# Optimization experiments

Hardware: AMD Instinct MI355X
Metric: run time of the kernel (lower is better)

The kernel has to match this reference:

```python
import jax, jax.numpy as jnp
import numpy as np

B, NR, NF, NH, NFH, D, HID = 32, 32, 128, 64, 64, 32, 256


def setup_inputs() -> dict:
    key = jax.random.key(0)
    ks = jax.random.split(key, 16)

    def w(k, o, i):
        return (jax.random.normal(k, (o, i), jnp.float32) / np.sqrt(i)).astype(jnp.float32)

    inp = {
        "robot": jax.random.normal(ks[0], (B, NR, D), jnp.float32),
        "frontier": jax.random.normal(ks[1], (B, NF, D), jnp.float32),
        "robot_history": jax.random.normal(ks[2], (B, NH, D), jnp.float32),
        "frontier_history": jax.random.normal(ks[3], (B, NFH, D), jnp.float32),
        "robot_frontier": jax.random.uniform(ks[4], (B, NR, NF), jnp.float32),
        "robot_past": jax.random.uniform(ks[5], (B, NR, NH), jnp.float32),
        "frontier_past": jax.random.uniform(ks[6], (B, NF, NFH), jnp.float32),
        # parameters (torch Linear convention: weight [out, in])
        "Wq": w(ks[7], D, D), "bq": jnp.zeros(D, jnp.float32),
        "Wk": w(ks[8], D, D), "bk": jnp.zeros(D, jnp.float32),
        "Wv": w(ks[9], D, D), "bv": jnp.zeros(D, jnp.float32),
        "Wn1": w(ks[10], HID, 2 * D), "bn1": jnp.zeros(HID, jnp.float32),
        "Wn2": w(ks[11], D, HID), "bn2": jnp.zeros(D, jnp.float32),
        "We1": w(ks[12], HID, 2 * D + 1), "be1": jnp.zeros(HID, jnp.float32),
        "We2": w(ks[13], 1, HID), "be2": jnp.zeros(1, jnp.float32),
    }
    return inp


def reference(robot, frontier, robot_history, frontier_history, robot_frontier,
              robot_past, frontier_past, Wq, bq, Wk, bk, Wv, bv,
              Wn1, bn1, Wn2, bn2, We1, be1, We2, be2):
    def lin(x, W, b):
        return x @ W.T + b

    def nmlp(h):
        return lin(jax.nn.relu(lin(h, Wn1, bn1)), Wn2, bn2)

    def emlp(h):
        return lin(jax.nn.relu(lin(h, We1, be1)), We2, be2)

    def intra(x):  # x: [b, n, D]
        q, k, v = lin(x, Wq, bq), lin(x, Wk, bk), lin(x, Wv, bv)
        e = jax.nn.softmax(jnp.einsum('bnd,bmd->bnm', q, k), axis=-1)
        agg = jnp.einsum('bnm,bmd->bnd', e, v)
        return x + nmlp(jnp.concatenate([x, agg], axis=-1))

    def inter(x, y, dis):  # x: [b,Nx,D], y: [b,Ny,D], dis: [b,Nx,Ny]
        xq, yk, yv = lin(x, Wq, bq), lin(y, Wk, bk), lin(y, Wv, bv)
        b, Nx, _ = x.shape
        Ny = y.shape[1]
        r_i = jnp.broadcast_to(xq[:, :, None, :], (b, Nx, Ny, D))
        f_j = jnp.broadcast_to(yk[:, None, :, :], (b, Nx, Ny, D))
        edge_input = jnp.concatenate([r_i, f_j, dis[..., None]], axis=-1)  # [b,Nx,Ny,65]
        score = emlp(edge_input)[..., 0]                                   # [b,Nx,Ny]
        e = jax.nn.softmax(score, axis=-1)
        agg = jnp.einsum('bnm,bmd->bnd', e, yv)
        x = x + nmlp(jnp.concatenate([x, agg], axis=-1))
        return e, x

    robot = intra(robot)
    frontier = intra(frontier)           # == per-sample intra on [1,Nf,D]
    robot_history = intra(robot_history)
    frontier_history = intra(frontier_history)
    _, robot = inter(robot, robot_history, robot_past)
    _, new_frontier = inter(frontier, frontier_history, frontier_past)
    edge, robot = inter(robot, new_frontier, robot_frontier)
    # original returns the intra-transformed frontier (split_frontier), not new_frontier
    return (robot, frontier, robot_history, frontier_history, edge)
```

## Files before the change

### kernel.cpp

```cpp
#include <hip/hip_runtime.h>

#define BATCH 32
#define NRr 32
#define NFf 128
#define NHh 64
#define NFHh 64
#define TI 4

__device__ __forceinline__ float dot4(float4 a, float4 b) {
    return fmaf(a.x, b.x, fmaf(a.y, b.y, fmaf(a.z, b.z, a.w * b.w)));
}

__global__ __launch_bounds__(256) void intra_kernel(
    const float* __restrict__ robot, const float* __restrict__ frontier,
    const float* __restrict__ rhist, const float* __restrict__ fhist,
    const float* __restrict__ Wq, const float* __restrict__ bq,
    const float* __restrict__ Wk, const float* __restrict__ bk,
    const float* __restrict__ Wv, const float* __restrict__ bv,
    const float* __restrict__ Wn1, const float* __restrict__ bn1,
    const float* __restrict__ Wn2, const float* __restrict__ bn2,
    float* __restrict__ o_robot, float* __restrict__ o_frontier,
    float* __restrict__ o_rh, float* __restrict__ o_fh)
{
    __shared__ __align__(16) float sXc[1024];
    __shared__ __align__(16) float sQ[1024];
    __shared__ __align__(16) float sAgg[1024];
    __shared__ __align__(16) float sS[4096];
    __shared__ __align__(16) float sKT[4128];
    __shared__ __align__(16) float sVT[8192];

    const int blk = blockIdx.x, tid = threadIdx.x;
    const float* xin; float* xout; int N, lgN, b, chunk;
    if (blk < 32)       { xin=robot;    xout=o_robot;    N=32;  lgN=5; b=blk;          chunk=0; }
    else if (blk < 160) { xin=frontier; xout=o_frontier; N=128; lgN=7; b=(blk-32)>>2;  chunk=(blk-32)&3; }
    else if (blk < 224) { xin=rhist;    xout=o_rh;       N=64;  lgN=6; b=(blk-160)>>1; chunk=(blk-160)&1; }
    else                { xin=fhist;    xout=o_fh;       N=64;  lgN=6; b=(blk-224)>>1; chunk=(blk-224)&1; }

    const float* xb = xin + (size_t)b * N * 32;
    const int r0 = chunk << 5;
    const int d = tid & 31;

    {
        int idx = tid;
        #pragma unroll
        for (int it = 0; it < 4; ++it, idx += 256)
            sXc[idx] = xb[(r0 << 5) + idx];
    }

    {
        const float4* wk4 = (const float4*)(Wk + (d << 5));
        const float4* wv4 = (const float4*)(Wv + (d << 5));
        float4 wk[8], wv[8];
        #pragma unroll
        for (int k = 0; k < 8; ++k) { wk[k] = wk4[k]; wv[k] = wv4[k]; }
        const float bkd = bk[d], bvd = bv[d];
        for (int idx = tid; idx < (N << 5); idx += 256) {
            int j = idx >> 5;
            const float4* xr = (const float4*)(xb + (j << 5));
            float aK = bkd, aV = bvd;
            #pragma unroll
            for (int k = 0; k < 8; ++k) {
                float4 xv = xr[k];
                aK += dot4(wk[k], xv);
                aV += dot4(wv[k], xv);
            }
            sKT[d * 129 + j] = aK;
            sVT[(j << 5) + d] = aV;
        }
    }
    __syncthreads();

    {
        const float4* wq4 = (const float4*)(Wq + (d << 5));
        float4 wq[8];
        #pragma unroll
        for (int k = 0; k < 8; ++k) wq[k] = wq4[k];
        const float bqd = bq[d];
        int idx = tid;
        #pragma unroll
        for (int it = 0; it < 4; ++it, idx += 256) {
            int r = idx >> 5;
            const float4* xr = (const float4*)(sXc + (r << 5));
            float a = bqd;
            #pragma unroll
            for (int k = 0; k < 8; ++k) a += dot4(wq[k], xr[k]);
            sQ[idx] = a;
        }
    }
    __syncthreads();

    for (int idx = tid; idx < (N << 5); idx += 256) {
        int r = idx >> lgN, j = idx & (N - 1);
        const float* qr = sQ + (r << 5);
        float a = 0.f;
        #pragma unroll
        for (int e = 0; e < 32; ++e) a = fmaf(qr[e], sKT[e * 129 + j], a);
        sS[idx] = a;
    }
    __syncthreads();

    {
        int r = tid >> 3, l = tid & 7;
        float* row = sS + (r << lgN);
        float m = -1e30f;
        for (int j = l; j < N; j += 8) m = fmaxf(m, row[j]);
        m = fmaxf(m, __shfl_xor(m, 4));
        m = fmaxf(m, __shfl_xor(m, 2));
        m = fmaxf(m, __shfl_xor(m, 1));
        float s = 0.f;
        for (int j = l; j < N; j += 8) { float ev = __expf(row[j] - m); row[j] = ev; s += ev; }
        s += __shfl_xor(s, 4); s += __shfl_xor(s, 2); s += __shfl_xor(s, 1);
        float inv = 1.0f / s;
        for (int j = l; j < N; j += 8) row[j] *= inv;
    }
    __syncthreads();

    {
        int idx = tid;
        #pragma unroll
        for (int it = 0; it < 4; ++it, idx += 256) {
            int r = idx >> 5;
            const float* er = sS + (r << lgN);
            float a = 0.f;
            for (int j = 0; j < N; ++j) a = fmaf(er[j], sVT[(j << 5) + d], a);
            sAgg[idx] = a;
        }
    }
    __syncthreads();

    float* sT = sVT;
    {
        const float4* w14 = (const float4*)(Wn1 + (tid << 6));
        float4 w1r[16];
        #pragma unroll
        for (int k = 0; k < 16; ++k) w1r[k] = w14[k];
        const float b1 = bn1[tid];
        for (int r = 0; r < 32; ++r) {
            const float4* xr = (const float4*)(sXc + (r << 5));
            const float4* ar = (const float4*)(sAgg + (r << 5));
            float a = b1;
            #pragma unroll
            for (int k = 0; k < 8; ++k) a += dot4(w1r[k], xr[k]);
            #pragma unroll
            for (int k = 0; k < 8; ++k) a += dot4(w1r[8 + k], ar[k]);
            sT[(r << 8) + tid] = fmaxf(a, 0.f);
        }
    }
    __syncthreads();

    {
        const int rg = tid >> 5;
        float acc[4] = {0.f, 0.f, 0.f, 0.f};
        #pragma unroll
        for (int hc = 0; hc < 4; ++hc) {
            const float4* w24 = (const float4*)(Wn2 + (d << 8) + (hc << 6));
            float4 w2r[16];
            #pragma unroll
            for (int k = 0; k < 16; ++k) w2r[k] = w24[k];
            #pragma unroll
            for (int p = 0; p < 4; ++p) {
                int r = rg + (p << 3);
                const float4* tr = (const float4*)(sT + (r << 8) + (hc << 6));
                float a = 0.f;
                #pragma unroll
                for (int k = 0; k < 16; ++k) a += dot4(w2r[k], tr[k]);
                acc[p] += a;
            }
        }
        const float b2 = bn2[d];
        #pragma unroll
        for (int p = 0; p < 4; ++p) {
            int r = rg + (p << 3);
            xout[((size_t)b * N << 5) + ((r0 + r) << 5) + d] = sXc[(r << 5) + d] + b2 + acc[p];
        }
    }
}

__global__ __launch_bounds__(256) void pre_y_kernel(
    const float* __restrict__ yA, int NyA, float* __restrict__ wOutA, float* __restrict__ yvOutA, int nBlkA,
    const float* __restrict__ yB, int NyB, float* __restrict__ wOutB, float* __restrict__ yvOutB,
    const float* __restrict__ Wk, const float* __restrict__ bk,
    const float* __restrict__ Wv, const float* __restrict__ bv,
    const float* __restrict__ We1)
{
    __shared__ __align__(16) float sY[256], sK[256];
    const int blk = blockIdx.x, tid = threadIdx.x;
    const float* y; int Ny; float* wOut; float* yvOut; int idx;
    if (blk < nBlkA) { y=yA; Ny=NyA; wOut=wOutA; yvOut=yvOutA; idx=blk; }
    else             { y=yB; Ny=NyB; wOut=wOutB; yvOut=yvOutB; idx=blk-nBlkA; }
    const int chunks = Ny >> 3;
    const int b = idx / chunks, j0 = (idx - b * chunks) << 3;

    sY[tid] = y[((size_t)(b * Ny + j0)) * 32 + tid];
    __syncthreads();

    {
        int jl = tid >> 5, dd = tid & 31;
        const float4* wk4 = (const float4*)(Wk + (dd << 5));
        const float4* wv4 = (const float4*)(Wv + (dd << 5));
        const float4* yr = (const float4*)(sY + (jl << 5));
        float aK = bk[dd], aV = bv[dd];
        #pragma unroll
        for (int k = 0; k < 8; ++k) {
            float4 yv4 = yr[k];
            aK += dot4(wk4[k], yv4);
            aV += dot4(wv4[k], yv4);
        }
        sK[(jl << 5) + dd] = aK;
        yvOut[((size_t)(b * Ny + j0 + jl)) * 32 + dd] = aV;
    }
    __syncthreads();

    {
        const float* w1 = We1 + tid * 65 + 32;
        float acc[8] = {0,0,0,0,0,0,0,0};
        #pragma unroll
        for (int e = 0; e < 32; ++e) {
            float we = w1[e];
            #pragma unroll
            for (int jl = 0; jl < 8; ++jl)
                acc[jl] = fmaf(we, sK[(jl << 5) + e], acc[jl]);
        }
        #pragma unroll
        for (int jl = 0; jl < 8; ++jl)
            wOut[((size_t)(b * Ny + j0 + jl)) * 256 + tid] = acc[jl];
    }
}

__global__ __launch_bounds__(256) void inter_main_kernel(
    const float* __restrict__ xA, int NxA, const float* __restrict__ wA, const float* __restrict__ yvA,
    int NyA, const float* __restrict__ disA, float* __restrict__ outA, float* __restrict__ eA, int nBlkA,
    const float* __restrict__ xB, int NxB, const float* __restrict__ wB, const float* __restrict__ yvB,
    int NyB, const float* __restrict__ disB, float* __restrict__ outB, float* __restrict__ eB,
    const float* __restrict__ Wq, const float* __restrict__ bq,
    const float* __restrict__ We1, const float* __restrict__ be1,
    const float* __restrict__ We2,
    const float* __restrict__ Wn1, const float* __restrict__ bn1,
    const float* __restrict__ Wn2, const float* __restrict__ bn2)
{
    __shared__ __align__(16) float sX[128], sQ[128], sAgg[128];
    __shared__ __align__(16) float sDis[512];
    __shared__ __align__(16) float sU[1024];
    __shared__ __align__(16) float sC[256], sW2[256];
    __shared__ __align__(16) float sS[512];
    __shared__ __align__(16) float sRed[1024];
    __shared__ __align__(16) float sT[1024];

    const int blk = blockIdx.x, tid = threadIdx.x;
    const float* x; int Nx; const float* w; const float* yv; int Ny;
    const float* dis; float* outp; float* ep; int idx;
    if (blk < nBlkA) { x=xA; Nx=NxA; w=wA; yv=yvA; Ny=NyA; dis=disA; outp=outA; ep=eA; idx=blk; }
    else             { x=xB; Nx=NxB; w=wB; yv=yvB; Ny=NyB; dis=disB; outp=outB; ep=eB; idx=blk-nBlkA; }
    const int lgNy = (Ny == 128) ? 7 : 6;
    const int tiles = Nx >> 2;
    const int b = idx / tiles, i0 = (idx - b * tiles) << 2;
    const float* xrow = x + ((size_t)(b * Nx + i0)) * 32;

    if (tid < 128) sX[tid] = xrow[tid];
    for (int k = tid; k < (TI << lgNy); k += 256) {
        int il = k >> lgNy, j = k & (Ny - 1);
        sDis[(il << 7) + j] = dis[((size_t)(b * Nx + i0 + il)) * Ny + j];
    }
    __syncthreads();

    if (tid < 128) {
        int il = tid >> 5, dd = tid & 31;
        const float4* wq4 = (const float4*)(Wq + (dd << 5));
        const float4* xr = (const float4*)(sX + (il << 5));
        float a = bq[dd];
        #pragma unroll
        for (int k = 0; k < 8; ++k) a += dot4(wq4[k], xr[k]);
        sQ[tid] = a;
    }
    __syncthreads();

    {
        const float* w1 = We1 + tid * 65;
        float acc[TI];
        const float b1 = be1[tid];
        #pragma unroll
        for (int il = 0; il < TI; ++il) acc[il] = b1;
        #pragma unroll
        for (int e = 0; e < 32; ++e) {
            float we = w1[e];
            #pragma unroll
            for (int il = 0; il < TI; ++il)
                acc[il] = fmaf(we, sQ[(il << 5) + e], acc[il]);
        }
        #pragma unroll
        for (int il = 0; il < TI; ++il) sU[(il << 8) + tid] = acc[il];
        sC[tid] = w1[64];
        sW2[tid] = We2[tid];
    }
    __syncthreads();

    {
        const int jg = tid >> 5, hh = tid & 31;
        for (int j = jg; j < Ny; j += 8) {
            const float* wr = w + ((size_t)(b * Ny + j)) * 256;
            float dv[TI];
            #pragma unroll
            for (int il = 0; il < TI; ++il) dv[il] = sDis[(il << 7) + j];
            float acc[TI] = {0.f, 0.f, 0.f, 0.f};
            #pragma unroll
            for (int h8 = 0; h8 < 8; ++h8) {
                int h = hh + (h8 << 5);
                float wv_ = wr[h];
                float c = sC[h], w2v = sW2[h];
                #pragma unroll
                for (int il = 0; il < TI; ++il) {
                    float hid = fmaf(c, dv[il], sU[(il << 8) + h] + wv_);
                    acc[il] = fmaf(w2v, fmaxf(hid, 0.f), acc[il]);
                }
            }
            #pragma unroll
            for (int m = 16; m; m >>= 1) {
                #pragma unroll
                for (int il = 0; il < TI; ++il) acc[il] += __shfl_xor(acc[il], m);
            }
            if (hh == 0) {
                #pragma unroll
                for (int il = 0; il < TI; ++il) sS[(il << 7) + j] = acc[il];
            }
        }
    }
    __syncthreads();

    {
        const int il = tid >> 6, lane = tid & 63;
        float m = -1e30f;
        for (int j = lane; j < Ny; j += 64) m = fmaxf(m, sS[(il << 7) + j]);
        #pragma unroll
        for (int msk = 32; msk; msk >>= 1) m = fmaxf(m, __shfl_xor(m, msk));
        float s = 0.f;
        for (int j = lane; j < Ny; j += 64) {
            float ev = __expf(sS[(il << 7) + j] - m);
            sS[(il << 7) + j] = ev; s += ev;
        }
        #pragma unroll
        for (int msk = 32; msk; msk >>= 1) s += __shfl_xor(s, msk);
        float inv = 1.0f / s;
        for (int j = lane; j < Ny; j += 64) sS[(il << 7) + j] *= inv;
    }
    __syncthreads();

    if (ep) {
        for (int k = tid; k < (TI << lgNy); k += 256) {
            int il = k >> lgNy, j = k & (Ny - 1);
            ep[((size_t)(b * Nx + i0 + il)) * Ny + j] = sS[(il << 7) + j];
        }
    }

    {
        const int jg = tid >> 5, dd = tid & 31;
        float p[TI] = {0.f, 0.f, 0.f, 0.f};
        for (int j = jg; j < Ny; j += 8) {
            float v = yv[((size_t)(b * Ny + j)) * 32 + dd];
            #pragma unroll
            for (int il = 0; il < TI; ++il)
                p[il] = fmaf(sS[(il << 7) + j], v, p[il]);
        }
        #pragma unroll
        for (int il = 0; il < TI; ++il) sRed[(jg << 7) + (il << 5) + dd] = p[il];
    }
    __syncthreads();
    if (tid < 128) {
        float a = 0.f;
        #pragma unroll
        for (int jg = 0; jg < 8; ++jg) a += sRed[(jg << 7) + tid];
        sAgg[tid] = a;
    }
    __syncthreads();

    {
        const float4* w14 = (const float4*)(Wn1 + (tid << 6));
        float acc[TI];
        const float b1 = bn1[tid];
        #pragma unroll
        for (int il = 0; il < TI; ++il) acc[il] = b1;
        #pragma unroll
        for (int k = 0; k < 8; ++k) {
            float4 wa = w14[k];
            #pragma unroll
            for (int il = 0; il < TI; ++il)
                acc[il] += dot4(wa, ((const float4*)(sX + (il << 5)))[k]);
        }
        #pragma unroll
        for (int k = 0; k < 8; ++k) {
            float4 wb = w14[8 + k];
            #pragma unroll
            for (int il = 0; il < TI; ++il)
                acc[il] += dot4(wb, ((const float4*)(sAgg + (il << 5)))[k]);
        }
        #pragma unroll
        for (int il = 0; il < TI; ++il) sT[(il << 8) + tid] = fmaxf(acc[il], 0.f);
    }
    __syncthreads();

    {
        const int hg = tid >> 5, dd = tid & 31;
        const float4* w24 = (const float4*)(Wn2 + (dd << 8) + (hg << 5));
        float p[TI] = {0.f, 0.f, 0.f, 0.f};
        #pragma unroll
        for (int k = 0; k < 8; ++k) {
            float4 wv_ = w24[k];
            #pragma unroll
            for (int il = 0; il < TI; ++il)
                p[il] += dot4(wv_, ((const float4*)(sT + (il << 8) + (hg << 5)))[k]);
        }
        #pragma unroll
        for (int il = 0; il < TI; ++il) sRed[(hg << 7) + (il << 5) + dd] = p[il];
    }
    __syncthreads();
    if (tid < 128) {
        int il = tid >> 5, dd = tid & 31;
        float a = bn2[dd] + sX[tid];
        #pragma unroll
        for (int hg = 0; hg < 8; ++hg) a += sRed[(hg << 7) + tid];
        outp[((size_t)(b * Nx + i0 + il)) * 32 + dd] = a;
    }
}

extern "C" void kernel_launch(void* const* d_in, const int* in_sizes, int n_in,
                              void* d_out, int out_size, void* d_ws, size_t ws_size,
                              hipStream_t stream) {
    const float* robot          = (const float*)d_in[0];
    const float* frontier       = (const float*)d_in[1];
    const float* rh             = (const float*)d_in[2];
    const float* fh             = (const float*)d_in[3];
    const float* robot_frontier = (const float*)d_in[4];
    const float* robot_past     = (const float*)d_in[5];
    const float* frontier_past  = (const float*)d_in[6];
    const float* Wq  = (const float*)d_in[7];  const float* bq  = (const float*)d_in[8];
    const float* Wk  = (const float*)d_in[9];  const float* bk  = (const float*)d_in[10];
    const float* Wv  = (const float*)d_in[11]; const float* bv  = (const float*)d_in[12];
    const float* Wn1 = (const float*)d_in[13]; const float* bn1 = (const float*)d_in[14];
    const float* Wn2 = (const float*)d_in[15]; const float* bn2 = (const float*)d_in[16];
    const float* We1 = (const float*)d_in[17]; const float* be1 = (const float*)d_in[18];
    const float* We2 = (const float*)d_in[19];

    float* out = (float*)d_out;
    float* out_robot    = out;
    float* out_frontier = out + 32768;
    float* out_rh       = out + 163840;
    float* out_fh       = out + 229376;
    float* out_edge     = out + 294912;

    float* W = (float*)d_ws;
    float* robot1 = W;
    float* robot2 = W + 32768;
    float* nf     = W + 65536;
    float* w5     = W + 196608;
    float* yv5    = W + 720896;
    float* w6     = W + 786432;
    float* yv6    = W + 1310720;
    float* w7     = W + 1376256;
    float* yv7    = W + 2424832;

    intra_kernel<<<288, 256, 0, stream>>>(robot, frontier, rh, fh,
        Wq, bq, Wk, bk, Wv, bv, Wn1, bn1, Wn2, bn2,
        robot1, out_frontier, out_rh, out_fh);

    pre_y_kernel<<<512, 256, 0, stream>>>(
        out_rh, NHh, w5, yv5, BATCH * NHh / 8,
        out_fh, NFHh, w6, yv6,
        Wk, bk, Wv, bv, We1);

    inter_main_kernel<<<1280, 256, 0, stream>>>(
        robot1, NRr, w5, yv5, NHh, robot_past, robot2, (float*)nullptr, BATCH * (NRr / TI),
        out_frontier, NFf, w6, yv6, NFHh, frontier_past, nf, (float*)nullptr,
        Wq, bq, We1, be1, We2, Wn1, bn1, Wn2, bn2);

    pre_y_kernel<<<512, 256, 0, stream>>>(
        nf, NFf, w7, yv7, BATCH * NFf / 8,
        nf, NFf, w7, yv7,
        Wk, bk, Wv, bv, We1);

    inter_main_kernel<<<256, 256, 0, stream>>>(
        robot2, NRr, w7, yv7, NFf, robot_frontier, out_robot, out_edge, BATCH * (NRr / TI),
        robot2, NRr, w7, yv7, NFf, robot_frontier, out_robot, out_edge,
        Wq, bq, We1, be1, We2, Wn1, bn1, Wn2, bn2);
}
```

Baseline: 223.7 us.

## Fuse key/value precompute into producer kernels and halve inter tile size

Removes both pre_y_kernel launches. The K/V projection and the We1 key contribution are now computed in the epilogue of the kernel that produces each tensor: intra_kernel for the history tensors, inter_main_kernel for new_frontier. The row tile TI drops from 4 to 2, doubling the inter grid and shrinking shared memory per block. The inner score loop now reads weight rows as float4 and keeps per-thread u/c/w2 values in registers. This saves two launches and a re-read of intermediates, at the cost of redundant weight loads per smaller tile and extra tail work in the producer blocks.

New measurement: 381.6 us. 1.71x slower.

```diff
diff --git a/kernel.cpp b/kernel.cpp
--- a/kernel.cpp
+++ b/kernel.cpp
@@ -5,7 +5,7 @@
 #define NFf 128
 #define NHh 64
 #define NFHh 64
-#define TI 4
+#define TI 2
 
 __device__ __forceinline__ float dot4(float4 a, float4 b) {
     return fmaf(a.x, b.x, fmaf(a.y, b.y, fmaf(a.z, b.z, a.w * b.w)));
@@ -19,8 +19,11 @@
     const float* __restrict__ Wv, const float* __restrict__ bv,
     const float* __restrict__ Wn1, const float* __restrict__ bn1,
     const float* __restrict__ Wn2, const float* __restrict__ bn2,
+    const float* __restrict__ We1,
     float* __restrict__ o_robot, float* __restrict__ o_frontier,
-    float* __restrict__ o_rh, float* __restrict__ o_fh)
+    float* __restrict__ o_rh, float* __restrict__ o_fh,
+    float* __restrict__ w5, float* __restrict__ yv5,
+    float* __restrict__ w6, float* __restrict__ yv6)
 {
     __shared__ __align__(16) float sXc[1024];
     __shared__ __align__(16) float sQ[1024];
@@ -31,10 +34,12 @@
 
     const int blk = blockIdx.x, tid = threadIdx.x;
     const float* xin; float* xout; int N, lgN, b, chunk;
+    float* wOut = nullptr; float* yvOut = nullptr;
     if (blk < 32)       { xin=robot;    xout=o_robot;    N=32;  lgN=5; b=blk;          chunk=0; }
     else if (blk < 160) { xin=frontier; xout=o_frontier; N=128; lgN=7; b=(blk-32)>>2;  chunk=(blk-32)&3; }
-    else if (blk < 224) { xin=rhist;    xout=o_rh;       N=64;  lgN=6; b=(blk-160)>>1; chunk=(blk-160)&1; }
-    else                { xin=fhist;    xout=o_fh;       N=64;  lgN=6; b=(blk-224)>>1; chunk=(blk-224)&1; }
+    else if (blk < 224) { xin=rhist;    xout=o_rh;       N=64;  lgN=6; b=(blk-160)>>1; chunk=(blk-160)&1; wOut=w5; yvOut=yv5; }
+    else                { xin=fhist;    xout=o_fh;       N=64;  lgN=6; b=(blk-224)>>1; chunk=(blk-224)&1; wOut=w6; yvOut=yv6; }
+    const bool isPre = (wOut != nullptr);
 
     const float* xb = xin + (size_t)b * N * 32;
     const int r0 = chunk << 5;
@@ -148,6 +153,7 @@
     }
     __syncthreads();
 
+    float* sOut = sQ;
     {
         const int rg = tid >> 5;
         float acc[4] = {0.f, 0.f, 0.f, 0.f};
@@ -171,99 +177,102 @@
         #pragma unroll
         for (int p = 0; p < 4; ++p) {
             int r = rg + (p << 3);
-            xout[((size_t)b * N << 5) + ((r0 + r) << 5) + d] = sXc[(r << 5) + d] + b2 + acc[p];
+            float v = sXc[(r << 5) + d] + b2 + acc[p];
+            xout[((size_t)b * N << 5) + ((r0 + r) << 5) + d] = v;
+            if (isPre) sOut[(r << 5) + d] = v;
+        }
+    }
+
+    if (isPre) {
+        __syncthreads();
+        float* sYK = sKT;
+        {
+            const float4* wk4 = (const float4*)(Wk + (d << 5));
+            const float4* wv4 = (const float4*)(Wv + (d << 5));
+            float4 wk[8], wv[8];
+            #pragma unroll
+            for (int k = 0; k < 8; ++k) { wk[k] = wk4[k]; wv[k] = wv4[k]; }
+            const float bkd = bk[d], bvd = bv[d];
+            const int rg = tid >> 5;
+            #pragma unroll
+            for (int p = 0; p < 4; ++p) {
+                int r = rg + (p << 3);
+                const float4* orow = (const float4*)(sOut + (r << 5));
+                float aK = bkd, aV = bvd;
+                #pragma unroll
+                for (int k = 0; k < 8; ++k) { aK += dot4(wk[k], orow[k]); aV += dot4(wv[k], orow[k]); }
+                sYK[r * 33 + d] = aK;
+                yvOut[(((size_t)(b * N + r0 + r)) << 5) + d] = aV;
+            }
+        }
+        __syncthreads();
+        {
+            const float* w1 = We1 + tid * 65 + 32;
+            #pragma unroll
+            for (int rc = 0; rc < 2; ++rc) {
+                float acc[16];
+                #pragma unroll
+                for (int r2 = 0; r2 < 16; ++r2) acc[r2] = 0.f;
+                #pragma unroll
+                for (int e = 0; e < 32; ++e) {
+                    float we = w1[e];
+                    #pragma unroll
+                    for (int r2 = 0; r2 < 16; ++r2)
+                        acc[r2] = fmaf(we, sYK[(rc * 16 + r2) * 33 + e], acc[r2]);
+                }
+                #pragma unroll
+                for (int r2 = 0; r2 < 16; ++r2)
+                    wOut[(((size_t)(b * N + r0 + rc * 16 + r2)) << 8) + tid] = acc[r2];
+            }
         }
     }
 }
 
-__global__ __launch_bounds__(256) void pre_y_kernel(
-    const float* __restrict__ yA, int NyA, float* __restrict__ wOutA, float* __restrict__ yvOutA, int nBlkA,
-    const float* __restrict__ yB, int NyB, float* __restrict__ wOutB, float* __restrict__ yvOutB,
+__global__ __launch_bounds__(256) void inter_main_kernel(
+    const float* __restrict__ xA, int NxA, const float* __restrict__ wA, const float* __restrict__ yvA,
+    int NyA, const float* __restrict__ disA, float* __restrict__ outA, float* __restrict__ eA,
+    float* __restrict__ wPreA, float* __restrict__ yvPreA, int nBlkA,
+    const float* __restrict__ xB, int NxB, const float* __restrict__ wB, const float* __restrict__ yvB,
+    int NyB, const float* __restrict__ disB, float* __restrict__ outB, float* __restrict__ eB,
+    float* __restrict__ wPreB, float* __restrict__ yvPreB,
+    const float* __restrict__ Wq, const float* __restrict__ bq,
     const float* __restrict__ Wk, const float* __restrict__ bk,
     const float* __restrict__ Wv, const float* __restrict__ bv,
-    const float* __restrict__ We1)
-{
-    __shared__ __align__(16) float sY[256], sK[256];
-    const int blk = blockIdx.x, tid = threadIdx.x;
-    const float* y; int Ny; float* wOut; float* yvOut; int idx;
-    if (blk < nBlkA) { y=yA; Ny=NyA; wOut=wOutA; yvOut=yvOutA; idx=blk; }
-    else             { y=yB; Ny=NyB; wOut=wOutB; yvOut=yvOutB; idx=blk-nBlkA; }
-    const int chunks = Ny >> 3;
-    const int b = idx / chunks, j0 = (idx - b * chunks) << 3;
-
-    sY[tid] = y[((size_t)(b * Ny + j0)) * 32 + tid];
-    __syncthreads();
-
-    {
-        int jl = tid >> 5, dd = tid & 31;
-        const float4* wk4 = (const float4*)(Wk + (dd << 5));
-        const float4* wv4 = (const float4*)(Wv + (dd << 5));
-        const float4* yr = (const float4*)(sY + (jl << 5));
-        float aK = bk[dd], aV = bv[dd];
-        #pragma unroll
-        for (int k = 0; k < 8; ++k) {
-            float4 yv4 = yr[k];
-            aK += dot4(wk4[k], yv4);
-            aV += dot4(wv4[k], yv4);
-        }
-        sK[(jl << 5) + dd] = aK;
-        yvOut[((size_t)(b * Ny + j0 + jl)) * 32 + dd] = aV;
-    }
-    __syncthreads();
-
-    {
-        const float* w1 = We1 + tid * 65 + 32;
-        float acc[8] = {0,0,0,0,0,0,0,0};
-        #pragma unroll
-        for (int e = 0; e < 32; ++e) {
-            float we = w1[e];
-            #pragma unroll
-            for (int jl = 0; jl < 8; ++jl)
-                acc[jl] = fmaf(we, sK[(jl << 5) + e], acc[jl]);
-        }
-        #pragma unroll
-        for (int jl = 0; jl < 8; ++jl)
-            wOut[((size_t)(b * Ny + j0 + jl)) * 256 + tid] = acc[jl];
-    }
-}
-
-__global__ __launch_bounds__(256) void inter_main_kernel(
-    const float* __restrict__ xA, int NxA, const float* __restrict__ wA, const float* __restrict__ yvA,
-    int NyA, const float* __restrict__ disA, float* __restrict__ outA, float* __restrict__ eA, int nBlkA,
-    const float* __restrict__ xB, int NxB, const float* __restrict__ wB, const float* __restrict__ yvB,
-    int NyB, const float* __restrict__ disB, float* __restrict__ outB, float* __restrict__ eB,
-    const float* __restrict__ Wq, const float* __restrict__ bq,
     const float* __restrict__ We1, const float* __restrict__ be1,
     const float* __restrict__ We2,
     const float* __restrict__ Wn1, const float* __restrict__ bn1,
     const float* __restrict__ Wn2, const float* __restrict__ bn2)
 {
-    __shared__ __align__(16) float sX[128], sQ[128], sAgg[128];
-    __shared__ __align__(16) float sDis[512];
-    __shared__ __align__(16) float sU[1024];
+    __shared__ __align__(16) float sX[64], sQ[64], sAgg[64], sOut[64];
+    __shared__ __align__(16) float sYK[66];
+    __shared__ __align__(16) float sDis[256];
+    __shared__ __align__(16) float sU[512];
     __shared__ __align__(16) float sC[256], sW2[256];
-    __shared__ __align__(16) float sS[512];
-    __shared__ __align__(16) float sRed[1024];
-    __shared__ __align__(16) float sT[1024];
+    __shared__ __align__(16) float sS[256];
+    __shared__ __align__(16) float sRed[512];
+    __shared__ __align__(16) float sT[512];
 
     const int blk = blockIdx.x, tid = threadIdx.x;
     const float* x; int Nx; const float* w; const float* yv; int Ny;
-    const float* dis; float* outp; float* ep; int idx;
-    if (blk < nBlkA) { x=xA; Nx=NxA; w=wA; yv=yvA; Ny=NyA; dis=disA; outp=outA; ep=eA; idx=blk; }
-    else             { x=xB; Nx=NxB; w=wB; yv=yvB; Ny=NyB; dis=disB; outp=outB; ep=eB; idx=blk-nBlkA; }
-    const int lgNy = (Ny == 128) ? 7 : 6;
-    const int tiles = Nx >> 2;
-    const int b = idx / tiles, i0 = (idx - b * tiles) << 2;
+    const float* dis; float* outp; float* ep; float* wPre; float* yvPre; int idx;
+    if (blk < nBlkA) { x=xA; Nx=NxA; w=wA; yv=yvA; Ny=NyA; dis=disA; outp=outA; ep=eA; wPre=wPreA; yvPre=yvPreA; idx=blk; }
+    else             { x=xB; Nx=NxB; w=wB; yv=yvB; Ny=NyB; dis=disB; outp=outB; ep=eB; wPre=wPreB; yvPre=yvPreB; idx=blk-nBlkA; }
+    const int tiles = Nx >> 1;
+    const int b = idx / tiles, i0 = (idx - b * tiles) << 1;
     const float* xrow = x + ((size_t)(b * Nx + i0)) * 32;
 
-    if (tid < 128) sX[tid] = xrow[tid];
-    for (int k = tid; k < (TI << lgNy); k += 256) {
-        int il = k >> lgNy, j = k & (Ny - 1);
-        sDis[(il << 7) + j] = dis[((size_t)(b * Nx + i0 + il)) * Ny + j];
-    }
-    __syncthreads();
-
-    if (tid < 128) {
+    if (tid < 64) sX[tid] = xrow[tid];
+    {
+        int per = Ny >> 2;
+        if (tid < (per << 1)) {
+            int il = (tid >= per) ? 1 : 0, jq = tid - il * per;
+            ((float4*)sDis)[(il << 5) + jq] =
+                ((const float4*)(dis + ((size_t)(b * Nx + i0 + il)) * Ny))[jq];
+        }
+    }
+    __syncthreads();
+
+    if (tid < 64) {
         int il = tid >> 5, dd = tid & 31;
         const float4* wq4 = (const float4*)(Wq + (dd << 5));
         const float4* xr = (const float4*)(sX + (il << 5));
@@ -276,19 +285,14 @@
 
     {
         const float* w1 = We1 + tid * 65;
-        float acc[TI];
-        const float b1 = be1[tid];
-        #pragma unroll
-        for (int il = 0; il < TI; ++il) acc[il] = b1;
+        float a0 = be1[tid], a1 = a0;
         #pragma unroll
         for (int e = 0; e < 32; ++e) {
             float we = w1[e];
-            #pragma unroll
-            for (int il = 0; il < TI; ++il)
-                acc[il] = fmaf(we, sQ[(il << 5) + e], acc[il]);
-        }
-        #pragma unroll
-        for (int il = 0; il < TI; ++il) sU[(il << 8) + tid] = acc[il];
+            a0 = fmaf(we, sQ[e], a0);
+            a1 = fmaf(we, sQ[32 + e], a1);
+        }
+        sU[tid] = a0; sU[256 + tid] = a1;
         sC[tid] = w1[64];
         sW2[tid] = We2[tid];
     }
@@ -296,128 +300,148 @@
 
     {
         const int jg = tid >> 5, hh = tid & 31;
+        float ur0[8], ur1[8], cr[8], w2r[8];
+        #pragma unroll
+        for (int k = 0; k < 8; ++k) {
+            int h = (hh << 3) + k;
+            cr[k] = sC[h]; w2r[k] = sW2[h];
+            ur0[k] = sU[h]; ur1[k] = sU[256 + h];
+        }
         for (int j = jg; j < Ny; j += 8) {
-            const float* wr = w + ((size_t)(b * Ny + j)) * 256;
-            float dv[TI];
-            #pragma unroll
-            for (int il = 0; il < TI; ++il) dv[il] = sDis[(il << 7) + j];
-            float acc[TI] = {0.f, 0.f, 0.f, 0.f};
-            #pragma unroll
-            for (int h8 = 0; h8 < 8; ++h8) {
-                int h = hh + (h8 << 5);
-                float wv_ = wr[h];
-                float c = sC[h], w2v = sW2[h];
-                #pragma unroll
-                for (int il = 0; il < TI; ++il) {
-                    float hid = fmaf(c, dv[il], sU[(il << 8) + h] + wv_);
-                    acc[il] = fmaf(w2v, fmaxf(hid, 0.f), acc[il]);
-                }
+            const float4* wr4 = (const float4*)(w + (((size_t)(b * Ny + j)) << 8) + (hh << 3));
+            float4 wa = wr4[0], wb = wr4[1];
+            float dv0 = sDis[j], dv1 = sDis[128 + j];
+            float wv8[8] = {wa.x, wa.y, wa.z, wa.w, wb.x, wb.y, wb.z, wb.w};
+            float a0 = 0.f, a1 = 0.f;
+            #pragma unroll
+            for (int k = 0; k < 8; ++k) {
+                float h0 = fmaf(cr[k], dv0, ur0[k] + wv8[k]);
+                float h1 = fmaf(cr[k], dv1, ur1[k] + wv8[k]);
+                a0 = fmaf(w2r[k], fmaxf(h0, 0.f), a0);
+                a1 = fmaf(w2r[k], fmaxf(h1, 0.f), a1);
             }
             #pragma unroll
             for (int m = 16; m; m >>= 1) {
-                #pragma unroll
-                for (int il = 0; il < TI; ++il) acc[il] += __shfl_xor(acc[il], m);
-            }
-            if (hh == 0) {
-                #pragma unroll
-                for (int il = 0; il < TI; ++il) sS[(il << 7) + j] = acc[il];
-            }
-        }
-    }
-    __syncthreads();
-
-    {
+                a0 += __shfl_xor(a0, m);
+                a1 += __shfl_xor(a1, m);
+            }
+            if (hh == 0) { sS[j] = a0; sS[128 + j] = a1; }
+        }
+    }
+    __syncthreads();
+
+    if (tid < 128) {
         const int il = tid >> 6, lane = tid & 63;
+        float* row = sS + (il << 7);
         float m = -1e30f;
-        for (int j = lane; j < Ny; j += 64) m = fmaxf(m, sS[(il << 7) + j]);
+        for (int j = lane; j < Ny; j += 64) m = fmaxf(m, row[j]);
         #pragma unroll
         for (int msk = 32; msk; msk >>= 1) m = fmaxf(m, __shfl_xor(m, msk));
         float s = 0.f;
-        for (int j = lane; j < Ny; j += 64) {
-            float ev = __expf(sS[(il << 7) + j] - m);
-            sS[(il << 7) + j] = ev; s += ev;
-        }
+        for (int j = lane; j < Ny; j += 64) { float ev = __expf(row[j] - m); row[j] = ev; s += ev; }
         #pragma unroll
         for (int msk = 32; msk; msk >>= 1) s += __shfl_xor(s, msk);
         float inv = 1.0f / s;
-        for (int j = lane; j < Ny; j += 64) sS[(il << 7) + j] *= inv;
+        for (int j = lane; j < Ny; j += 64) row[j] *= inv;
     }
     __syncthreads();
 
     if (ep) {
-        for (int k = tid; k < (TI << lgNy); k += 256) {
-            int il = k >> lgNy, j = k & (Ny - 1);
-            ep[((size_t)(b * Nx + i0 + il)) * Ny + j] = sS[(il << 7) + j];
+        for (int k = tid; k < (TI * 128) && (k >> 7) < TI; k += 256) {
+            int il = k >> 7, j = k & 127;
+            if (j < Ny) ep[((size_t)(b * Nx + i0 + il)) * Ny + j] = sS[(il << 7) + j];
         }
     }
 
     {
         const int jg = tid >> 5, dd = tid & 31;
-        float p[TI] = {0.f, 0.f, 0.f, 0.f};
+        float p0 = 0.f, p1 = 0.f;
         for (int j = jg; j < Ny; j += 8) {
-            float v = yv[((size_t)(b * Ny + j)) * 32 + dd];
-            #pragma unroll
-            for (int il = 0; il < TI; ++il)
-                p[il] = fmaf(sS[(il << 7) + j], v, p[il]);
-        }
-        #pragma unroll
-        for (int il = 0; il < TI; ++il) sRed[(jg << 7) + (il << 5) + dd] = p[il];
-    }
-    __syncthreads();
-    if (tid < 128) {
+            float v = yv[(((size_t)(b * Ny + j)) << 5) + dd];
+            p0 = fmaf(sS[j], v, p0);
+            p1 = fmaf(sS[128 + j], v, p1);
+        }
+        sRed[(jg << 6) + dd] = p0;
+        sRed[(jg << 6) + 32 + dd] = p1;
+    }
+    __syncthreads();
+    if (tid < 64) {
         float a = 0.f;
         #pragma unroll
-        for (int jg = 0; jg < 8; ++jg) a += sRed[(jg << 7) + tid];
+        for (int jg = 0; jg < 8; ++jg) a += sRed[(jg << 6) + tid];
         sAgg[tid] = a;
     }
     __syncthreads();
 
     {
         const float4* w14 = (const float4*)(Wn1 + (tid << 6));
-        float acc[TI];
-        const float b1 = bn1[tid];
-        #pragma unroll
-        for (int il = 0; il < TI; ++il) acc[il] = b1;
+        float a0 = bn1[tid], a1 = a0;
         #pragma unroll
         for (int k = 0; k < 8; ++k) {
             float4 wa = w14[k];
-            #pragma unroll
-            for (int il = 0; il < TI; ++il)
-                acc[il] += dot4(wa, ((const float4*)(sX + (il << 5)))[k]);
+            a0 += dot4(wa, ((const float4*)sX)[k]);
+            a1 += dot4(wa, ((const float4*)(sX + 32))[k]);
         }
         #pragma unroll
         for (int k = 0; k < 8; ++k) {
             float4 wb = w14[8 + k];
-            #pragma unroll
-            for (int il = 0; il < TI; ++il)
-                acc[il] += dot4(wb, ((const float4*)(sAgg + (il << 5)))[k]);
-        }
-        #pragma unroll
-        for (int il = 0; il < TI; ++il) sT[(il << 8) + tid] = fmaxf(acc[il], 0.f);
+            a0 += dot4(wb, ((const float4*)sAgg)[k]);
+            a1 += dot4(wb, ((const float4*)(sAgg + 32))[k]);
+        }
+        sT[tid] = fmaxf(a0, 0.f);
+        sT[256 + tid] = fmaxf(a1, 0.f);
     }
     __syncthreads();
 
     {
         const int hg = tid >> 5, dd = tid & 31;
         const float4* w24 = (const float4*)(Wn2 + (dd << 8) + (hg << 5));
-        float p[TI] = {0.f, 0.f, 0.f, 0.f};
+        float p0 = 0.f, p1 = 0.f;
         #pragma unroll
         for (int k = 0; k < 8; ++k) {
-            float4 wv_ = w24[k];
-            #pragma unroll
-            for (int il = 0; il < TI; ++il)
-                p[il] += dot4(wv_, ((const float4*)(sT + (il << 8) + (hg << 5)))[k]);
-        }
-        #pragma unroll
-        for (int il = 0; il < TI; ++il) sRed[(hg << 7) + (il << 5) + dd] = p[il];
-    }
-    __syncthreads();
-    if (tid < 128) {
+            float4 wv4 = w24[k];
+            p0 += dot4(wv4, ((const float4*)(sT + (hg << 5)))[k]);
+            p1 += dot4(wv4, ((const float4*)(sT + 256 + (hg << 5)))[k]);
+        }
+        sRed[(hg << 6) + dd] = p0;
+        sRed[(hg << 6) + 32 + dd] = p1;
+    }
+    __syncthreads();
+    if (tid < 64) {
         int il = tid >> 5, dd = tid & 31;
         float a = bn2[dd] + sX[tid];
         #pragma unroll
-        for (int hg = 0; hg < 8; ++hg) a += sRed[(hg << 7) + tid];
+        for (int hg = 0; hg < 8; ++hg) a += sRed[(hg << 6) + tid];
         outp[((size_t)(b * Nx + i0 + il)) * 32 + dd] = a;
+        sOut[tid] = a;
+    }
+
+    if (wPre) {
+        __syncthreads();
+        if (tid < 128) {
+            int half = tid >> 6, t = tid & 63;
+            int il = t >> 5, dd = t & 31;
+            const float4* wm4 = (const float4*)((half ? Wv : Wk) + (dd << 5));
+            const float4* orow = (const float4*)(sOut + (il << 5));
+            float a = half ? bv[dd] : bk[dd];
+            #pragma unroll
+            for (int k = 0; k < 8; ++k) a += dot4(wm4[k], orow[k]);
+            if (half) yvPre[(((size_t)(b * Nx + i0 + il)) << 5) + dd] = a;
+            else sYK[il * 33 + dd] = a;
+        }
+        __syncthreads();
+        {
+            const float* w1 = We1 + tid * 65 + 32;
+            float a0 = 0.f, a1 = 0.f;
+            #pragma unroll
+            for (int e = 0; e < 32; ++e) {
+                float we = w1[e];
+                a0 = fmaf(we, sYK[e], a0);
+                a1 = fmaf(we, sYK[33 + e], a1);
+            }
+            wPre[(((size_t)(b * Nx + i0)) << 8) + tid] = a0;
+            wPre[(((size_t)(b * Nx + i0 + 1)) << 8) + tid] = a1;
+        }
     }
 }
 
@@ -458,26 +482,20 @@
     float* yv7    = W + 2424832;
 
     intra_kernel<<<288, 256, 0, stream>>>(robot, frontier, rh, fh,
-        Wq, bq, Wk, bk, Wv, bv, Wn1, bn1, Wn2, bn2,
-        robot1, out_frontier, out_rh, out_fh);
-
-    pre_y_kernel<<<512, 256, 0, stream>>>(
-        out_rh, NHh, w5, yv5, BATCH * NHh / 8,
-        out_fh, NFHh, w6, yv6,
-        Wk, bk, Wv, bv, We1);
-
-    inter_main_kernel<<<1280, 256, 0, stream>>>(
-        robot1, NRr, w5, yv5, NHh, robot_past, robot2, (float*)nullptr, BATCH * (NRr / TI),
-        out_frontier, NFf, w6, yv6, NFHh, frontier_past, nf, (float*)nullptr,
-        Wq, bq, We1, be1, We2, Wn1, bn1, Wn2, bn2);
-
-    pre_y_kernel<<<512, 256, 0, stream>>>(
-        nf, NFf, w7, yv7, BATCH * NFf / 8,
-        nf, NFf, w7, yv7,
-        Wk, bk, Wv, bv, We1);
-
-    inter_main_kernel<<<256, 256, 0, stream>>>(
-        robot2, NRr, w7, yv7, NFf, robot_frontier, out_robot, out_edge, BATCH * (NRr / TI),
+        Wq, bq, Wk, bk, Wv, bv, Wn1, bn1, Wn2, bn2, We1,
+        robot1, out_frontier, out_rh, out_fh, w5, yv5, w6, yv6);
+
+    inter_main_kernel<<<2560, 256, 0, stream>>>(
+        robot1, NRr, w5, yv5, NHh, robot_past, robot2,
+        (float*)nullptr, (float*)nullptr, (float*)nullptr, BATCH * (NRr / TI),
+        out_frontier, NFf, w6, yv6, NFHh, frontier_past, nf,
+        (float*)nullptr, w7, yv7,
+        Wq, bq, Wk, bk, Wv, bv, We1, be1, We2, Wn1, bn1, Wn2, bn2);
+
+    inter_main_kernel<<<512, 256, 0, stream>>>(
         robot2, NRr, w7, yv7, NFf, robot_frontier, out_robot, out_edge,
-        Wq, bq, We1, be1, We2, Wn1, bn1, Wn2, bn2);
+        (float*)nullptr, (float*)nullptr, BATCH * (NRr / TI),
+        robot2, NRr, w7, yv7, NFf, robot_frontier, out_robot, out_edge,
+        (float*)nullptr, (float*)nullptr,
+        Wq, bq, Wk, bk, Wv, bv, We1, be1, We2, Wn1, bn1, Wn2, bn2);
 }
```

## Transpose edge-weight buffer layout and remap score loop to per-lane neighbors

Applied to the files above, without the earlier changes.

The precomputed per-neighbor hidden projection is now written in a [b][h/4][Ny][4] interleaved layout. The score kernel assigns one wave per query row and one lane per neighbor, reading float4 chunks coalesced across lanes, which removes the cross-lane shuffle reductions. Softmax, the edge output write and aggregation are folded into per-wave code with fewer barriers, and the distance row load is vectorized. Each lane now runs a serial 256-long hidden loop, and the producer kernel's stores become strided.

Result: slower. 250.9 us (+12.2%).

```diff
diff --git a/kernel.cpp b/kernel.cpp
--- a/kernel.cpp
+++ b/kernel.cpp
@@ -221,9 +221,10 @@
             for (int jl = 0; jl < 8; ++jl)
                 acc[jl] = fmaf(we, sK[(jl << 5) + e], acc[jl]);
         }
+        float* wbase = wOut + (((size_t)b * 64 + (tid >> 2)) * Ny + j0) * 4 + (tid & 3);
         #pragma unroll
         for (int jl = 0; jl < 8; ++jl)
-            wOut[((size_t)(b * Ny + j0 + jl)) * 256 + tid] = acc[jl];
+            wbase[jl << 2] = acc[jl];
     }
 }
 
@@ -257,9 +258,10 @@
     const float* xrow = x + ((size_t)(b * Nx + i0)) * 32;
 
     if (tid < 128) sX[tid] = xrow[tid];
-    for (int k = tid; k < (TI << lgNy); k += 256) {
-        int il = k >> lgNy, j = k & (Ny - 1);
-        sDis[(il << 7) + j] = dis[((size_t)(b * Nx + i0 + il)) * Ny + j];
+    if (tid < Ny) {
+        int il = tid >> (lgNy - 2), jq = tid & ((Ny >> 2) - 1);
+        ((float4*)sDis)[(il << 5) + jq] =
+            ((const float4*)(dis + ((size_t)(b * Nx + i0 + il)) * Ny))[jq];
     }
     __syncthreads();
 
@@ -276,8 +278,8 @@
 
     {
         const float* w1 = We1 + tid * 65;
+        const float b1 = be1[tid];
         float acc[TI];
-        const float b1 = be1[tid];
         #pragma unroll
         for (int il = 0; il < TI; ++il) acc[il] = b1;
         #pragma unroll
@@ -294,88 +296,86 @@
     }
     __syncthreads();
 
-    {
-        const int jg = tid >> 5, hh = tid & 31;
-        for (int j = jg; j < Ny; j += 8) {
-            const float* wr = w + ((size_t)(b * Ny + j)) * 256;
-            float dv[TI];
-            #pragma unroll
-            for (int il = 0; il < TI; ++il) dv[il] = sDis[(il << 7) + j];
-            float acc[TI] = {0.f, 0.f, 0.f, 0.f};
-            #pragma unroll
-            for (int h8 = 0; h8 < 8; ++h8) {
-                int h = hh + (h8 << 5);
-                float wv_ = wr[h];
-                float c = sC[h], w2v = sW2[h];
-                #pragma unroll
-                for (int il = 0; il < TI; ++il) {
-                    float hid = fmaf(c, dv[il], sU[(il << 8) + h] + wv_);
-                    acc[il] = fmaf(w2v, fmaxf(hid, 0.f), acc[il]);
-                }
+    const int wv = tid >> 6, lane = tid & 63;
+    {
+        const float4* wT4 = (const float4*)w + (size_t)(b * 64) * Ny;
+        const float4* u4p = (const float4*)(sU + (wv << 8));
+        const float4* c4p = (const float4*)sC;
+        const float4* p4p = (const float4*)sW2;
+        if (Ny == 64) {
+            float dv = sDis[(wv << 7) + lane];
+            float acc = 0.f;
+            #pragma unroll 8
+            for (int hc = 0; hc < 64; ++hc) {
+                float4 wv4 = wT4[(size_t)hc * 64 + lane];
+                float4 u4 = u4p[hc], c4 = c4p[hc], p4 = p4p[hc];
+                acc = fmaf(p4.x, fmaxf(fmaf(c4.x, dv, u4.x + wv4.x), 0.f), acc);
+                acc = fmaf(p4.y, fmaxf(fmaf(c4.y, dv, u4.y + wv4.y), 0.f), acc);
+                acc = fmaf(p4.z, fmaxf(fmaf(c4.z, dv, u4.z + wv4.z), 0.f), acc);
+                acc = fmaf(p4.w, fmaxf(fmaf(c4.w, dv, u4.w + wv4.w), 0.f), acc);
             }
-            #pragma unroll
-            for (int m = 16; m; m >>= 1) {
-                #pragma unroll
-                for (int il = 0; il < TI; ++il) acc[il] += __shfl_xor(acc[il], m);
+            sS[(wv << 7) + lane] = acc;
+        } else {
+            float dv0 = sDis[(wv << 7) + lane];
+            float dv1 = sDis[(wv << 7) + 64 + lane];
+            float acc0 = 0.f, acc1 = 0.f;
+            #pragma unroll 4
+            for (int hc = 0; hc < 64; ++hc) {
+                float4 wa = wT4[(size_t)hc * 128 + lane];
+                float4 wb = wT4[(size_t)hc * 128 + 64 + lane];
+                float4 u4 = u4p[hc], c4 = c4p[hc], p4 = p4p[hc];
+                acc0 = fmaf(p4.x, fmaxf(fmaf(c4.x, dv0, u4.x + wa.x), 0.f), acc0);
+                acc0 = fmaf(p4.y, fmaxf(fmaf(c4.y, dv0, u4.y + wa.y), 0.f), acc0);
+                acc0 = fmaf(p4.z, fmaxf(fmaf(c4.z, dv0, u4.z + wa.z), 0.f), acc0);
+                acc0 = fmaf(p4.w, fmaxf(fmaf(c4.w, dv0, u4.w + wa.w), 0.f), acc0);
+                acc1 = fmaf(p4.x, fmaxf(fmaf(c4.x, dv1, u4.x + wb.x), 0.f), acc1);
+                acc1 = fmaf(p4.y, fmaxf(fmaf(c4.y, dv1, u4.y + wb.y), 0.f), acc1);
+                acc1 = fmaf(p4.z, fmaxf(fmaf(c4.z, dv1, u4.z + wb.z), 0.f), acc1);
+                acc1 = fmaf(p4.w, fmaxf(fmaf(c4.w, dv1, u4.w + wb.w), 0.f), acc1);
             }
-            if (hh == 0) {
-                #pragma unroll
-                for (int il = 0; il < TI; ++il) sS[(il << 7) + j] = acc[il];
-            }
-        }
-    }
-    __syncthreads();
-
-    {
-        const int il = tid >> 6, lane = tid & 63;
-        float m = -1e30f;
-        for (int j = lane; j < Ny; j += 64) m = fmaxf(m, sS[(il << 7) + j]);
+            sS[(wv << 7) + lane] = acc0;
+            sS[(wv << 7) + 64 + lane] = acc1;
+        }
+    }
+    __syncthreads();
+
+    {
+        float v0 = sS[(wv << 7) + lane];
+        float v1 = (Ny == 128) ? sS[(wv << 7) + 64 + lane] : -1e30f;
+        float m = fmaxf(v0, v1);
         #pragma unroll
         for (int msk = 32; msk; msk >>= 1) m = fmaxf(m, __shfl_xor(m, msk));
-        float s = 0.f;
-        for (int j = lane; j < Ny; j += 64) {
-            float ev = __expf(sS[(il << 7) + j] - m);
-            sS[(il << 7) + j] = ev; s += ev;
-        }
+        float e0 = __expf(v0 - m);
+        float e1 = (Ny == 128) ? __expf(v1 - m) : 0.f;
+        float s = e0 + e1;
         #pragma unroll
         for (int msk = 32; msk; msk >>= 1) s += __shfl_xor(s, msk);
         float inv = 1.0f / s;
-        for (int j = lane; j < Ny; j += 64) sS[(il << 7) + j] *= inv;
-    }
-    __syncthreads();
-
-    if (ep) {
-        for (int k = tid; k < (TI << lgNy); k += 256) {
-            int il = k >> lgNy, j = k & (Ny - 1);
-            ep[((size_t)(b * Nx + i0 + il)) * Ny + j] = sS[(il << 7) + j];
-        }
-    }
-
-    {
-        const int jg = tid >> 5, dd = tid & 31;
-        float p[TI] = {0.f, 0.f, 0.f, 0.f};
-        for (int j = jg; j < Ny; j += 8) {
-            float v = yv[((size_t)(b * Ny + j)) * 32 + dd];
-            #pragma unroll
-            for (int il = 0; il < TI; ++il)
-                p[il] = fmaf(sS[(il << 7) + j], v, p[il]);
-        }
-        #pragma unroll
-        for (int il = 0; il < TI; ++il) sRed[(jg << 7) + (il << 5) + dd] = p[il];
-    }
-    __syncthreads();
-    if (tid < 128) {
-        float a = 0.f;
-        #pragma unroll
-        for (int jg = 0; jg < 8; ++jg) a += sRed[(jg << 7) + tid];
-        sAgg[tid] = a;
+        e0 *= inv; e1 *= inv;
+        sS[(wv << 7) + lane] = e0;
+        if (Ny == 128) sS[(wv << 7) + 64 + lane] = e1;
+        if (ep) {
+            float* erow = ep + ((size_t)(b * Nx + i0 + wv)) * Ny;
+            erow[lane] = e0;
+            if (Ny == 128) erow[64 + lane] = e1;
+        }
+    }
+    __syncthreads();
+
+    {
+        const int dd = lane & 31, jg = lane >> 5;
+        float p = 0.f;
+        for (int j = jg; j < Ny; j += 2)
+            p = fmaf(sS[(wv << 7) + j], yv[(((size_t)(b * Ny + j)) << 5) + dd], p);
+        p += __shfl_xor(p, 32);
+        if (jg == 0) sAgg[(wv << 5) + dd] = p;
     }
     __syncthreads();
 
     {
         const float4* w14 = (const float4*)(Wn1 + (tid << 6));
+        const float b1 = bn1[tid];
         float acc[TI];
-        const float b1 = bn1[tid];
         #pragma unroll
         for (int il = 0; il < TI; ++il) acc[il] = b1;
         #pragma unroll
@@ -400,13 +400,15 @@
     {
         const int hg = tid >> 5, dd = tid & 31;
         const float4* w24 = (const float4*)(Wn2 + (dd << 8) + (hg << 5));
+        float4 w2r[8];
+        #pragma unroll
+        for (int k = 0; k < 8; ++k) w2r[k] = w24[k];
         float p[TI] = {0.f, 0.f, 0.f, 0.f};
         #pragma unroll
         for (int k = 0; k < 8; ++k) {
-            float4 wv_ = w24[k];
             #pragma unroll
             for (int il = 0; il < TI; ++il)
-                p[il] += dot4(wv_, ((const float4*)(sT + (il << 8) + (hg << 5)))[k]);
+                p[il] += dot4(w2r[k], ((const float4*)(sT + (il << 8) + (hg << 5)))[k]);
         }
         #pragma unroll
         for (int il = 0; il < TI; ++il) sRed[(hg << 7) + (il << 5) + dd] = p[il];
```
